# Optimization experiments

Hardware: AMD Instinct MI355X
Metric: run time of the kernel (lower is better)

Reference implementation:

```python
import jax, jax.numpy as jnp
import numpy as np


def setup_inputs() -> dict:
    key = jax.random.key(0)
    k1, k2 = jax.random.split(key)
    N, L, Q, H, Lv, P = 1, 6, 300, 8, 4, 4
    # FPN levels for an 800x1333 image at strides 8/16/32/64 (H, W per level)
    spatial_shapes = np.array([[100, 167], [50, 84], [25, 42], [13, 21]], dtype=np.int64)
    level_start_index = np.concatenate([[0], np.cumsum(spatial_shapes.prod(1))[:-1]]).astype(np.int64)
    sampling_locations = jax.random.uniform(k1, (N, L, Q, H, Lv, P, 2), dtype=jnp.float32)
    # attention weights normalized over (levels*points) per head, as MSDeformAttn produces
    aw = jax.random.normal(k2, (N, L, Q, H, Lv, P), dtype=jnp.float32)
    attention_weights = jax.nn.softmax(aw.reshape(N, L, Q, H, Lv * P), axis=-1).reshape(N, L, Q, H, Lv, P)
    return dict(sampling_locations=sampling_locations,
                attention_weights=attention_weights,
                spatial_shapes=spatial_shapes,
                level_start_index=level_start_index)


def reference(sampling_locations, attention_weights, spatial_shapes, level_start_index):
    # sampling_locations: (N, L, Q, H, Lv, P, 2); attention_weights: (N, L, Q, H, Lv, P)
    N, L, Q, H, Lv, P, _ = sampling_locations.shape
    S = int(np.sum(np.asarray(spatial_shapes)[:, 0] * np.asarray(spatial_shapes)[:, 1]))  # static
    ss = jnp.asarray(spatial_shapes)          # (Lv, 2) = (H, W)
    lsi = jnp.asarray(level_start_index)      # (Lv,)

    # permute(0,1,3,2,5,4,6).flatten(0,3) -> (M, P, Lv, 2) with M = N*L*H*Q
    sl = jnp.transpose(sampling_locations, (0, 1, 3, 2, 5, 4, 6)).reshape(-1, P, Lv, 2)
    aw = jnp.transpose(attention_weights, (0, 1, 3, 2, 5, 4)).reshape(-1, P, Lv)
    M = aw.shape[0]

    rev = ss[:, ::-1].astype(sl.dtype)        # (Lv, 2) = (W, H)
    crf = sl * rev                            # float (col, row) coords, (M, P, Lv, 2)
    crll = jnp.floor(crf)
    f = crf - crll                            # fractional part, (M, P, Lv, 2)
    fc, fr = f[..., 0], f[..., 1]

    # corners (d_col, d_row) paired with their bilinear margins (matches torch zipped order)
    offsets = jnp.array([[0, 0], [0, 1], [1, 0], [1, 1]], dtype=jnp.int32)  # ll, lh, hl, hh
    margins = jnp.stack([(fc - 1.0) * (fr - 1.0),   # margin_hh for corner ll
                         -(fc - 1.0) * fr,           # margin_hl for corner lh
                         -fc * (fr - 1.0),           # margin_lh for corner hl
                         fc * fr], axis=0)           # margin_ll for corner hh  -> (4, M, P, Lv)

    cri = crll.astype(jnp.int32)[None] + offsets[:, None, None, None, :]    # (4, M, P, Lv, 2)
    Wlv = ss[:, 1].astype(jnp.int32)
    Hlv = ss[:, 0].astype(jnp.int32)
    valid = ((cri[..., 0] >= 0) & (cri[..., 0] < Wlv) &
             (cri[..., 1] >= 0) & (cri[..., 1] < Hlv))                       # (4, M, P, Lv)

    idx = (cri[..., 1] * Wlv + cri[..., 0] + lsi.astype(jnp.int32)) * valid  # invalid -> 0
    w = aw[None] * valid * margins                                           # invalid -> 0 weight

    # single fused scatter-add over all 4 corners
    idx_flat = jnp.moveaxis(idx, 0, 1).reshape(M, -1)   # (M, 4*P*Lv)
    w_flat = jnp.moveaxis(w, 0, 1).reshape(M, -1)
    rows = jnp.arange(M)[:, None]
    flat_grid = jnp.zeros((M, S), dtype=jnp.float32).at[rows, idx_flat].add(w_flat)

    # torch: reshape(N, Len_q, n_layers, n_heads, -1).sum((2,3)).permute(0,2,1)
    return jnp.transpose(flat_grid.reshape(N, Q, L, H, S).sum(axis=(2, 3)), (0, 2, 1))
```

## Files before the change

kernel.cpp:

```cpp
#include <hip/hip_runtime.h>


constexpr int NQ   = 300;
constexpr int QW   = 8;
constexpr int NG   = 38;
constexpr int NTILES = 14;
constexpr int MAXC = 2016;
constexpr int BLK  = 512;

__global__ __launch_bounds__(BLK)
void msda_tiled(const float2* __restrict__ loc,
                const float*  __restrict__ aw,
                float*        __restrict__ out) {
    __shared__ float sm[QW * MAXC];

    const int b  = blockIdx.x;
    const int g  = b / NTILES;
    const int tb = b % NTILES;

    int lv, r0t, nr;
    if (tb < 9)       { lv = 0; r0t = 12 * tb;        nr = min(12, 100 - r0t); }
    else if (tb < 12) { lv = 1; r0t = 24 * (tb - 9);  nr = min(24, 50  - r0t); }
    else if (tb < 13) { lv = 2; r0t = 0;              nr = 25; }
    else              { lv = 3; r0t = 0;              nr = 13; }

    const int Wlv_[4] = {167, 84, 42, 21};
    const int Hlv_[4] = {100, 50, 25, 13};
    const int lsi_[4] = {0, 16700, 20900, 21950};
    const int W    = Wlv_[lv];
    const int base = lsi_[lv];
    const int g0   = g * QW;
    const int qw   = min(QW, NQ - g0);
    const int cells = nr * W;
    const int tid  = threadIdx.x;

    float4* sm4 = (float4*)sm;
    for (int i = tid; i < QW * MAXC / 4; i += BLK) sm4[i] = make_float4(0.f, 0.f, 0.f, 0.f);
    __syncthreads();

    const int nm4 = 48 * qw * 4;
    const int rlo = r0t, rhi = r0t + nr;
    const float fW = (float)W, fH = (float)Hlv_[lv];
    const int m0 = 48 * g0;

    for (int i = tid; i < nm4; i += BLK) {
        const int mi = i >> 2, p = i & 3;
        const int m  = m0 + mi;
        const int ql = mi / 48;
        const int l  = m / 2400;
        const int rem = m - l * 2400;
        const int h  = rem / 300;
        const int q  = rem - h * 300;
        const int t  = (((l * 300 + q) * 8 + h) * 4 + lv) * 4 + p;

        const float2 xy = loc[t];
        const float  w  = aw[t];

        const float cf  = xy.x * fW;
        const float rf  = xy.y * fH;
        const float cfl = floorf(cf), rfl = floorf(rf);
        const float fc  = cf - cfl, fr = rf - rfl;
        const int c0 = (int)cfl, rr = (int)rfl;
        const int c1 = c0 + 1, r1 = rr + 1;

        const bool cv0 = (unsigned)c0 < (unsigned)W;
        const bool cv1 = (unsigned)c1 < (unsigned)W;
        const bool rv0 = (rr >= rlo) & (rr < rhi);
        const bool rv1 = (r1 >= rlo) & (r1 < rhi);

        const float omfc = 1.0f - fc, omfr = 1.0f - fr;
        float* smq = &sm[ql * MAXC];
        if (rv0) {
            const int ro = (rr - rlo) * W;
            if (cv0) atomicAdd(&smq[ro + c0], w * omfc * omfr);
            if (cv1) atomicAdd(&smq[ro + c1], w * fc   * omfr);
        }
        if (rv1) {
            const int ro = (r1 - rlo) * W;
            if (cv0) atomicAdd(&smq[ro + c0], w * omfc * fr);
            if (cv1) atomicAdd(&smq[ro + c1], w * fc   * fr);
        }
    }
    __syncthreads();

    const int s0  = base + r0t * W;
    const int nq4 = qw >> 2;
    for (int i = tid; i < cells * nq4; i += BLK) {
        const int cell = i / nq4;
        const int v    = i - cell * nq4;
        float4 val;
        val.x = sm[(v * 4 + 0) * MAXC + cell];
        val.y = sm[(v * 4 + 1) * MAXC + cell];
        val.z = sm[(v * 4 + 2) * MAXC + cell];
        val.w = sm[(v * 4 + 3) * MAXC + cell];
        *(float4*)&out[(s0 + cell) * NQ + g0 + v * 4] = val;
    }
}

extern "C" void kernel_launch(void* const* d_in, const int* in_sizes, int n_in,
                              void* d_out, int out_size, void* d_ws, size_t ws_size,
                              hipStream_t stream) {
    const float2* loc = (const float2*)d_in[0];
    const float*  aw  = (const float*)d_in[1];
    float* out = (float*)d_out;

    msda_tiled<<<NG * NTILES, BLK, 0, stream>>>(loc, aw, out);
}
```

Before: 82.72 us.

## Use smaller row tiles, vectorize point loads, and zero only used shared memory

```diff
diff --git a/kernel.cpp b/kernel.cpp
--- a/kernel.cpp
+++ b/kernel.cpp
@@ -4,13 +4,13 @@
 constexpr int NQ   = 300;
 constexpr int QW   = 8;
 constexpr int NG   = 38;
-constexpr int NTILES = 14;
-constexpr int MAXC = 2016;
+constexpr int NTILES = 21;
+constexpr int MAXC = 1280;
 constexpr int BLK  = 512;
 
-__global__ __launch_bounds__(BLK)
-void msda_tiled(const float2* __restrict__ loc,
-                const float*  __restrict__ aw,
+__global__ __launch_bounds__(BLK, 8)
+void msda_tiled(const float4* __restrict__ loc4,
+                const float4* __restrict__ aw4,
                 float*        __restrict__ out) {
     __shared__ float sm[QW * MAXC];
 
@@ -19,9 +19,9 @@
     const int tb = b % NTILES;
 
     int lv, r0t, nr;
-    if (tb < 9)       { lv = 0; r0t = 12 * tb;        nr = min(12, 100 - r0t); }
-    else if (tb < 12) { lv = 1; r0t = 24 * (tb - 9);  nr = min(24, 50  - r0t); }
-    else if (tb < 13) { lv = 2; r0t = 0;              nr = 25; }
+    if (tb < 15)      { lv = 0; r0t = 7  * tb;        nr = min(7,  100 - r0t); }
+    else if (tb < 19) { lv = 1; r0t = 15 * (tb - 15); nr = min(15, 50  - r0t); }
+    else if (tb < 20) { lv = 2; r0t = 0;              nr = 25; }
     else              { lv = 3; r0t = 0;              nr = 13; }
 
     const int Wlv_[4] = {167, 84, 42, 21};
@@ -34,51 +34,62 @@
     const int cells = nr * W;
     const int tid  = threadIdx.x;
 
-    float4* sm4 = (float4*)sm;
-    for (int i = tid; i < QW * MAXC / 4; i += BLK) sm4[i] = make_float4(0.f, 0.f, 0.f, 0.f);
+    {
+        const int nz = qw * (MAXC / 4);
+        float4* sm4 = (float4*)sm;
+        for (int i = tid; i < nz; i += BLK) sm4[i] = make_float4(0.f, 0.f, 0.f, 0.f);
+    }
     __syncthreads();
 
-    const int nm4 = 48 * qw * 4;
+    const int nm  = 48 * qw;
     const int rlo = r0t, rhi = r0t + nr;
     const float fW = (float)W, fH = (float)Hlv_[lv];
-    const int m0 = 48 * g0;
 
-    for (int i = tid; i < nm4; i += BLK) {
-        const int mi = i >> 2, p = i & 3;
-        const int m  = m0 + mi;
+    if (tid < nm) {
+        const int mi = tid;
+        const int m  = 48 * g0 + mi;
         const int ql = mi / 48;
         const int l  = m / 2400;
         const int rem = m - l * 2400;
         const int h  = rem / 300;
         const int q  = rem - h * 300;
-        const int t  = (((l * 300 + q) * 8 + h) * 4 + lv) * 4 + p;
+        const int t  = (((l * 300 + q) * 8 + h) * 4 + lv) * 4;
 
-        const float2 xy = loc[t];
-        const float  w  = aw[t];
+        const float4 xy01 = loc4[(t >> 1) + 0];
+        const float4 xy23 = loc4[(t >> 1) + 1];
+        const float4 w4   = aw4[t >> 2];
 
-        const float cf  = xy.x * fW;
-        const float rf  = xy.y * fH;
-        const float cfl = floorf(cf), rfl = floorf(rf);
-        const float fc  = cf - cfl, fr = rf - rfl;
-        const int c0 = (int)cfl, rr = (int)rfl;
-        const int c1 = c0 + 1, r1 = rr + 1;
+        float* smq = &sm[ql * MAXC];
 
-        const bool cv0 = (unsigned)c0 < (unsigned)W;
-        const bool cv1 = (unsigned)c1 < (unsigned)W;
-        const bool rv0 = (rr >= rlo) & (rr < rhi);
-        const bool rv1 = (r1 >= rlo) & (r1 < rhi);
+        #pragma unroll
+        for (int p = 0; p < 4; ++p) {
+            const float x = (p == 0) ? xy01.x : (p == 1) ? xy01.z : (p == 2) ? xy23.x : xy23.z;
+            const float y = (p == 0) ? xy01.y : (p == 1) ? xy01.w : (p == 2) ? xy23.y : xy23.w;
+            const float w = (p == 0) ? w4.x   : (p == 1) ? w4.y   : (p == 2) ? w4.z   : w4.w;
 
-        const float omfc = 1.0f - fc, omfr = 1.0f - fr;
-        float* smq = &sm[ql * MAXC];
-        if (rv0) {
-            const int ro = (rr - rlo) * W;
-            if (cv0) atomicAdd(&smq[ro + c0], w * omfc * omfr);
-            if (cv1) atomicAdd(&smq[ro + c1], w * fc   * omfr);
-        }
-        if (rv1) {
-            const int ro = (r1 - rlo) * W;
-            if (cv0) atomicAdd(&smq[ro + c0], w * omfc * fr);
-            if (cv1) atomicAdd(&smq[ro + c1], w * fc   * fr);
+            const float cf  = x * fW;
+            const float rf  = y * fH;
+            const float cfl = floorf(cf), rfl = floorf(rf);
+            const float fc  = cf - cfl, fr = rf - rfl;
+            const int c0 = (int)cfl, rr = (int)rfl;
+            const int c1 = c0 + 1, r1 = rr + 1;
+
+            const bool cv0 = (unsigned)c0 < (unsigned)W;
+            const bool cv1 = (unsigned)c1 < (unsigned)W;
+            const bool rv0 = (rr >= rlo) & (rr < rhi);
+            const bool rv1 = (r1 >= rlo) & (r1 < rhi);
+
+            const float omfc = 1.0f - fc, omfr = 1.0f - fr;
+            if (rv0) {
+                const int ro = (rr - rlo) * W;
+                if (cv0) atomicAdd(&smq[ro + c0], w * omfc * omfr);
+                if (cv1) atomicAdd(&smq[ro + c1], w * fc   * omfr);
+            }
+            if (rv1) {
+                const int ro = (r1 - rlo) * W;
+                if (cv0) atomicAdd(&smq[ro + c0], w * omfc * fr);
+                if (cv1) atomicAdd(&smq[ro + c1], w * fc   * fr);
+            }
         }
     }
     __syncthreads();
@@ -100,9 +111,9 @@
 extern "C" void kernel_launch(void* const* d_in, const int* in_sizes, int n_in,
                               void* d_out, int out_size, void* d_ws, size_t ws_size,
                               hipStream_t stream) {
-    const float2* loc = (const float2*)d_in[0];
-    const float*  aw  = (const float*)d_in[1];
+    const float4* loc4 = (const float4*)d_in[0];
+    const float4* aw4  = (const float4*)d_in[1];
     float* out = (float*)d_out;
 
-    msda_tiled<<<NG * NTILES, BLK, 0, stream>>>(loc, aw, out);
+    msda_tiled<<<NG * NTILES, BLK, 0, stream>>>(loc4, aw4, out);
 }
```

After: 79.95 us, median of 3. -3.4%, faster.
